# Performance work log

Hardware: AMD Instinct MI355X
Metric: run time of the kernel (lower is better)

The kernel has to match this reference:

```python
import jax, jax.numpy as jnp
import numpy as np

N_NODES = 100000
N_REL = 8
N_EDGES = 400000
D = 128
N_LAYERS = 3
NEG_SLOPE = 0.2


def setup_inputs() -> dict:
    key = jax.random.key(0)
    ks = jax.random.split(key, 8)
    scale = 0.05
    return {
        "h": jax.random.normal(ks[0], (N_NODES, D), dtype=jnp.float32),
        "edge_src": jax.random.randint(ks[1], (N_REL, N_EDGES), 0, N_NODES, dtype=jnp.int32),
        "edge_dst": jax.random.randint(ks[2], (N_REL, N_EDGES), 0, N_NODES, dtype=jnp.int32),
        "fc_src_w": jax.random.normal(ks[3], (N_LAYERS, N_REL, D, D), dtype=jnp.float32) * scale,
        "fc_dst_w": jax.random.normal(ks[4], (N_LAYERS, N_REL, D, D), dtype=jnp.float32) * scale,
        "attn_l": jax.random.normal(ks[5], (N_LAYERS, N_REL, D), dtype=jnp.float32) * scale,
        "attn_r": jax.random.normal(ks[6], (N_LAYERS, N_REL, D), dtype=jnp.float32) * scale,
        "h_bias": jax.random.normal(ks[7], (N_LAYERS, D), dtype=jnp.float32) * scale,
    }


def _rel_graph_layer(x, edge_src, edge_dst, Wsrc, Wdst, al, ar, bias, apply_relu):
    """One RelGraphConvLayer: per-relation GATConv (1 head) summed across relations."""
    n = x.shape[0]
    out = jnp.zeros((n, Wsrc.shape[-2]), dtype=x.dtype)
    for r in range(edge_src.shape[0]):
        src, dst = edge_src[r], edge_dst[r]
        zs = x @ Wsrc[r].T                      # [N, D] fc_src projection
        zd = x @ Wdst[r].T                      # [N, D] fc_dst projection
        el = zs @ al[r]                         # [N]
        er = zd @ ar[r]                         # [N]
        e = jax.nn.leaky_relu(el[src] + er[dst], NEG_SLOPE)  # [E]
        # edge softmax over incoming edges per dst node (stable)
        m = jax.ops.segment_max(e, dst, num_segments=n)
        w = jnp.exp(e - m[dst])
        denom = jax.ops.segment_sum(w, dst, num_segments=n)
        alpha = w / denom[dst]                  # [E]
        msg = zs[src] * alpha[:, None]          # [E, D]
        out = out + jax.ops.segment_sum(msg, dst, num_segments=n)
    out = out + bias
    if apply_relu:
        out = jax.nn.relu(out)
    return out  # mean over single head dim is a no-op


def reference(h, edge_src, edge_dst, fc_src_w, fc_dst_w, attn_l, attn_r, h_bias):
    x = h
    for l in range(N_LAYERS):
        x = _rel_graph_layer(
            x, edge_src, edge_dst,
            fc_src_w[l], fc_dst_w[l], attn_l[l], attn_r[l], h_bias[l],
            apply_relu=(l < N_LAYERS - 1),
        )
    return x
```

## Files before the change

kernel.cpp:

```cpp
#include <hip/hip_runtime.h>

#define NN 100000
#define NE 400000
#define NR 8
#define DD 128
#define NBK 391
#define BCAP 1536
#define P1B 32
#define NNP 100096

typedef unsigned short ushort_t;
using short8  = __attribute__((ext_vector_type(8))) short;
using f32x4   = __attribute__((ext_vector_type(4))) float;

__device__ __forceinline__ ushort_t f2bf(float f) {
  union { float f; unsigned u; } v; v.f = f;
  unsigned u = v.u;
  return (ushort_t)((u + 0x7FFFu + ((u >> 16) & 1u)) >> 16);
}
__device__ __forceinline__ float bf2f(unsigned hs) {
  union { unsigned u; float f; } v; v.u = hs << 16;
  return v.f;
}

__global__ __launch_bounds__(256) void f32_to_bf16_kernel(const float* __restrict__ in,
                                                          ushort_t* __restrict__ out, int n4) {
  int t = blockIdx.x * 256 + threadIdx.x;
  if (t < n4) {
    float4 f = ((const float4*)in)[t];
    uint2 p;
    p.x = (unsigned)f2bf(f.x) | ((unsigned)f2bf(f.y) << 16);
    p.y = (unsigned)f2bf(f.z) | ((unsigned)f2bf(f.w) << 16);
    ((uint2*)out)[t] = p;
  }
}

__global__ __launch_bounds__(256) void wfrag_kernel(const float* __restrict__ in, uint4* __restrict__ out) {
  int t = blockIdx.x * 256 + threadIdx.x;
  int lane = t & 63;
  int nt = (t >> 6) & 7;
  int s  = (t >> 9) & 3;
  int kc = (t >> 11) & 7;
  int l  = t >> 14;
  int m16 = lane & 15, kq = lane >> 4;
  int o = nt * 16 + m16;
  int chunk = s * 4 + kq;
  const float* p = in + ((((size_t)l * 8 + kc) * 128 + o) * 128 + chunk * 8);
  uint4 v;
  v.x = (unsigned)f2bf(p[0]) | ((unsigned)f2bf(p[1]) << 16);
  v.y = (unsigned)f2bf(p[2]) | ((unsigned)f2bf(p[3]) << 16);
  v.z = (unsigned)f2bf(p[4]) | ((unsigned)f2bf(p[5]) << 16);
  v.w = (unsigned)f2bf(p[6]) | ((unsigned)f2bf(p[7]) << 16);
  out[t] = v;
}

__global__ __launch_bounds__(256) void bucket_kernel(const int* __restrict__ edge_dst,
                                                     const int* __restrict__ edge_src,
                                                     int* __restrict__ gcur, unsigned* __restrict__ E1) {
  __shared__ unsigned stage[NBK][32];
  __shared__ int lcnt[NBK];
  int r   = blockIdx.x >> 5;
  int blk = blockIdx.x & 31;
  int t = threadIdx.x;
  for (int i = t; i < NBK; i += 256) lcnt[i] = 0;
  __syncthreads();
  const int per = NE / P1B;
  int e0 = blk * per, e1 = e0 + per;
  const int* ed = edge_dst + (size_t)r * NE;
  const int* es = edge_src + (size_t)r * NE;
  int* gc = gcur + r * NBK;
  unsigned* E1r = E1 + (size_t)r * NBK * BCAP;
  for (int base = e0; base < e1; base += 4096) {
    int lim = min(base + 4096, e1);
    for (int e = base + t; e < lim; e += 256) {
      int d = ed[e];
      unsigned val = ((unsigned)es[e] << 8) | (unsigned)(d & 255);
      int b = d >> 8;
      int slot = atomicAdd(&lcnt[b], 1);
      if (slot < 32) stage[b][slot] = val;
      else {
        int p = atomicAdd(&gc[b], 1);
        if (p < BCAP) E1r[(size_t)b * BCAP + p] = val;
      }
    }
    __syncthreads();
    for (int b = t; b < NBK; b += 256) {
      int c = lcnt[b]; if (c > 32) c = 32;
      int nf = c & ~15;
      if (nf) {
        int p = atomicAdd(&gc[b], nf);
        for (int k = 0; k < nf; k++)
          if (p + k < BCAP) E1r[(size_t)b * BCAP + p + k] = stage[b][k];
        for (int k = nf; k < c; k++) stage[b][k - nf] = stage[b][k];
      }
      lcnt[b] = c - nf;
    }
    __syncthreads();
  }
  for (int b = t; b < NBK; b += 256) {
    int c = lcnt[b]; if (c > 32) c = 32;
    if (c) {
      int p = atomicAdd(&gc[b], c);
      for (int k = 0; k < c; k++)
        if (p + k < BCAP) E1r[(size_t)b * BCAP + p + k] = stage[b][k];
    }
  }
}

__global__ __launch_bounds__(256) void bscan_kernel(const int* __restrict__ gcur, int* __restrict__ bbase) {
  __shared__ int ps[256];
  int t = threadIdx.x;
  int vals[13];
  int s = 0;
#pragma unroll
  for (int i = 0; i < 13; i++) {
    int idx = t * 13 + i;
    int c = (idx < NR * NBK) ? min(gcur[idx], BCAP) : 0;
    vals[i] = s; s += c;
  }
  ps[t] = s;
  __syncthreads();
  for (int off = 1; off < 256; off <<= 1) {
    int x = (t >= off) ? ps[t - off] : 0;
    __syncthreads();
    ps[t] += x;
    __syncthreads();
  }
  int excl = ps[t] - s;
#pragma unroll
  for (int i = 0; i < 13; i++) {
    int idx = t * 13 + i;
    if (idx < NR * NBK) bbase[idx] = excl + vals[i];
  }
}

__global__ __launch_bounds__(256) void csr_kernel(const unsigned* __restrict__ E1, const int* __restrict__ gcur,
                                                  const int* __restrict__ bbase,
                                                  int* __restrict__ offs, int* __restrict__ srcs) {
  __shared__ unsigned ent[BCAP];
  __shared__ int cnt[256], pref[256], excl_s[256];
  int rb = blockIdx.x;
  int b = rb % NBK, r = rb / NBK;
  int t = threadIdx.x;
  int n = min(gcur[rb], BCAP);
  const unsigned* src = E1 + (size_t)rb * BCAP;
  for (int i = t; i < n; i += 256) ent[i] = src[i];
  cnt[t] = 0;
  __syncthreads();
  for (int i = t; i < n; i += 256) atomicAdd(&cnt[ent[i] & 255], 1);
  __syncthreads();
  int v = cnt[t];
  pref[t] = v;
  __syncthreads();
  for (int off = 1; off < 256; off <<= 1) {
    int x = (t >= off) ? pref[t - off] : 0;
    __syncthreads();
    pref[t] += x;
    __syncthreads();
  }
  int excl = pref[t] - v;
  excl_s[t] = excl;
  int gb = bbase[rb];
  int d = b * 256 + t;
  if (d < NN) offs[(size_t)r * NN + d] = gb + excl;
  if (rb == NR * NBK - 1 && t == 0) offs[(size_t)NR * NN] = NR * NE;
  cnt[t] = 0;
  __syncthreads();
  for (int i = t; i < n; i += 256) {
    unsigned e = ent[i];
    int dl = e & 255;
    int p = atomicAdd(&cnt[dl], 1);
    srcs[gb + excl_s[dl] + p] = (int)(e >> 8);
  }
}

__global__ __launch_bounds__(128) void uv_all_kernel(const float* __restrict__ Wsrc, const float* __restrict__ Wdst,
                                                     const float* __restrict__ al, const float* __restrict__ ar,
                                                     ushort_t* __restrict__ uvb) {
  int rl = blockIdx.x, j = threadIdx.x;
  int l = rl >> 3, r = rl & 7;
  const float* Ws = Wsrc + (size_t)rl * DD * DD;
  const float* Wd = Wdst + (size_t)rl * DD * DD;
  float su = 0.f, sv = 0.f;
  for (int i = 0; i < DD; i++) {
    su += al[rl * DD + i] * Ws[i * DD + j];
    sv += ar[rl * DD + i] * Wd[i * DD + j];
  }
  uvb[((size_t)l * 16 + r) * DD + j]     = f2bf(su);
  uvb[((size_t)l * 16 + 8 + r) * DD + j] = f2bf(sv);
}

__global__ __launch_bounds__(256) void elr_kernel(const ushort_t* __restrict__ xb,
                                                  const ushort_t* __restrict__ uvb,
                                                  float* __restrict__ elr) {
  int t = threadIdx.x;
  int lane = t & 63, wave = t >> 6;
  int m16 = lane & 15, kq = lane >> 4;
  int n0 = blockIdx.x * 64 + wave * 16;
  const short8* Ag = (const short8*)xb;
  const short8* Bg = (const short8*)uvb;
  int bbase = m16 * 16 + kq;
  short8 b0 = Bg[bbase + 0];
  short8 b1 = Bg[bbase + 4];
  short8 b2 = Bg[bbase + 8];
  short8 b3 = Bg[bbase + 12];
  size_t abase = (size_t)(n0 + m16) * 16 + kq;
  short8 a0 = Ag[abase + 0];
  short8 a1 = Ag[abase + 4];
  short8 a2 = Ag[abase + 8];
  short8 a3 = Ag[abase + 12];
  f32x4 acc = (f32x4)(0.f);
  acc = __builtin_amdgcn_mfma_f32_16x16x32_bf16(a0, b0, acc, 0, 0, 0);
  acc = __builtin_amdgcn_mfma_f32_16x16x32_bf16(a1, b1, acc, 0, 0, 0);
  acc = __builtin_amdgcn_mfma_f32_16x16x32_bf16(a2, b2, acc, 0, 0, 0);
  acc = __builtin_amdgcn_mfma_f32_16x16x32_bf16(a3, b3, acc, 0, 0, 0);
#pragma unroll
  for (int i = 0; i < 4; i++) {
    int n = n0 + kq * 4 + i;
    if (n < NN) elr[(size_t)m16 * NN + n] = acc[i];
  }
}

#define GACC(J, P, W) { g##J[0] += (W) * bf2f((P).x & 0xffffu); g##J[1] += (W) * bf2f((P).x >> 16); \
                        g##J[2] += (W) * bf2f((P).y & 0xffffu); g##J[3] += (W) * bf2f((P).y >> 16); \
                        g##J[4] += (W) * bf2f((P).z & 0xffffu); g##J[5] += (W) * bf2f((P).z >> 16); \
                        g##J[6] += (W) * bf2f((P).w & 0xffffu); g##J[7] += (W) * bf2f((P).w >> 16); }

__global__ __launch_bounds__(256, 4) void agg_gemm_kernel(
    const int* __restrict__ srcs, const int* __restrict__ offs,
    const float* __restrict__ el, const float* __restrict__ er,
    const ushort_t* __restrict__ xin, const uint4* __restrict__ Wfrag,
    const float* __restrict__ bias, ushort_t* __restrict__ xout,
    float* __restrict__ dout, int relu, int last) {
  int t = threadIdx.x;
  int lane = t & 63, wave = t >> 6;
  int m16 = lane & 15, kq = lane >> 4;
  int row0 = blockIdx.x * 64;
  int n = row0 + wave * 16 + m16;
  const uint4* xk = (const uint4*)xin + kq;
  f32x4 acc[8];
#pragma unroll
  for (int nt = 0; nt < 8; nt++) acc[nt] = (f32x4)(0.f);

#pragma unroll 1
  for (int kc = 0; kc < NR; kc++) {
    float g0[8], g1[8], g2[8], g3[8];
#pragma unroll
    for (int c = 0; c < 8; c++) { g0[c] = 0.f; g1[c] = 0.f; g2[c] = 0.f; g3[c] = 0.f; }
    if (n < NN) {
      int k0 = offs[(size_t)kc * NN + n], k1 = offs[(size_t)kc * NN + n + 1];
      if (k1 > k0) {
        float erd = er[(size_t)kc * NN + n];
        const float* elv = el + (size_t)kc * NN;
        float denom = 0.f;
        for (int e = k0; e < k1; e += 2) {
          int s0 = srcs[e];
          int s1 = srcs[(e + 1 < k1) ? e + 1 : e];
          const uint4* q0 = xk + (size_t)s0 * 16;
          const uint4* q1 = xk + (size_t)s1 * 16;
          uint4 p00 = q0[0], p01 = q0[4], p02 = q0[8], p03 = q0[12];
          uint4 p10 = q1[0], p11 = q1[4], p12 = q1[8], p13 = q1[12];
          float x0 = elv[s0] + erd;
          float x1 = elv[s1] + erd;
          x0 = fmaxf(x0, 0.2f * x0);
          x1 = fmaxf(x1, 0.2f * x1);
          float w0 = __expf(x0);
          float w1 = (e + 1 < k1) ? __expf(x1) : 0.f;
          denom += w0 + w1;
          GACC(0, p00, w0) GACC(1, p01, w0) GACC(2, p02, w0) GACC(3, p03, w0)
          GACC(0, p10, w1) GACC(1, p11, w1) GACC(2, p12, w1) GACC(3, p13, w1)
        }
        float inv = 1.f / denom;
#pragma unroll
        for (int c = 0; c < 8; c++) { g0[c] *= inv; g1[c] *= inv; g2[c] *= inv; g3[c] *= inv; }
      }
    }
    short8 af[4];
#pragma unroll
    for (int c = 0; c < 8; c++) {
      af[0][c] = (short)f2bf(g0[c]);
      af[1][c] = (short)f2bf(g1[c]);
      af[2][c] = (short)f2bf(g2[c]);
      af[3][c] = (short)f2bf(g3[c]);
    }
    const uint4* wfp = Wfrag + (size_t)kc * 2048 + lane;
#pragma unroll
    for (int s = 0; s < 4; s++) {
#pragma unroll
      for (int nt = 0; nt < 8; nt++) {
        short8 bf = *reinterpret_cast<const short8*>(wfp + (s * 8 + nt) * 64);
        acc[nt] = __builtin_amdgcn_mfma_f32_16x16x32_bf16(af[s], bf, acc[nt], 0, 0, 0);
      }
    }
  }
#pragma unroll
  for (int i = 0; i < 4; i++) {
    int row = row0 + wave * 16 + kq * 4 + i;
    if (row < NN) {
#pragma unroll
      for (int nt = 0; nt < 8; nt++) {
        float vv = acc[nt][i] + bias[m16 + 16 * nt];
        if (relu) vv = fmaxf(vv, 0.f);
        if (last) dout[(size_t)row * DD + m16 + 16 * nt] = vv;
        else      xout[(size_t)row * DD + m16 + 16 * nt] = f2bf(vv);
      }
    }
  }
}

extern "C" void kernel_launch(void* const* d_in, const int* in_sizes, int n_in,
                              void* d_out, int out_size, void* d_ws, size_t ws_size,
                              hipStream_t stream) {
  const float* h        = (const float*)d_in[0];
  const int*   edge_src = (const int*)d_in[1];
  const int*   edge_dst = (const int*)d_in[2];
  const float* fc_src_w = (const float*)d_in[3];
  const float* fc_dst_w = (const float*)d_in[4];
  const float* attn_l   = (const float*)d_in[5];
  const float* attn_r   = (const float*)d_in[6];
  const float* h_bias   = (const float*)d_in[7];
  float* dout = (float*)d_out;
  (void)in_sizes; (void)n_in; (void)out_size; (void)ws_size;

  char* base = (char*)d_ws;
  size_t off = 0;
  auto alloc = [&](size_t bytes) -> void* {
    void* p = base + off;
    off += (bytes + 255) & ~(size_t)255;
    return p;
  };
  ushort_t* xb0   = (ushort_t*)alloc((size_t)NNP * DD * 2);
  ushort_t* xb1   = (ushort_t*)alloc((size_t)NNP * DD * 2);
  float*    ELR   = (float*)   alloc((size_t)16 * NN * 4);
  ushort_t* uvb   = (ushort_t*)alloc((size_t)3 * 16 * DD * 2);
  uint4*    Wfrag = (uint4*)   alloc((size_t)3 * NR * 4 * 8 * 64 * 16);
  int*      offs  = (int*)     alloc(((size_t)NR * NN + 1) * 4);
  unsigned* E1    = (unsigned*)alloc((size_t)NR * NBK * BCAP * 4);
  int*      gcur  = (int*)     alloc((size_t)NR * NBK * 4);
  int*      bbase = (int*)     alloc((size_t)NR * NBK * 4);
  int*      srcs  = (int*)     alloc((size_t)NR * NE * 4);

  (void)hipMemsetAsync(gcur, 0, (size_t)NR * NBK * 4, stream);
  (void)hipMemsetAsync(xb0 + (size_t)NN * DD, 0, (size_t)(NNP - NN) * DD * 2, stream);
  (void)hipMemsetAsync(xb1 + (size_t)NN * DD, 0, (size_t)(NNP - NN) * DD * 2, stream);
  bucket_kernel<<<NR * P1B, 256, 0, stream>>>(edge_dst, edge_src, gcur, E1);
  bscan_kernel<<<1, 256, 0, stream>>>(gcur, bbase);
  csr_kernel<<<NR * NBK, 256, 0, stream>>>(E1, gcur, bbase, offs, srcs);

  f32_to_bf16_kernel<<<(NN * DD / 4 + 255) / 256, 256, 0, stream>>>(h, xb0, NN * DD / 4);
  wfrag_kernel<<<3 * NR * 4 * 8 * 64 / 256, 256, 0, stream>>>(fc_src_w, Wfrag);
  uv_all_kernel<<<3 * NR, 128, 0, stream>>>(fc_src_w, fc_dst_w, attn_l, attn_r, uvb);

  const float* el = ELR;
  const float* er = ELR + (size_t)8 * NN;
  for (int l = 0; l < 3; l++) {
    ushort_t* xin  = (l & 1) ? xb1 : xb0;
    ushort_t* xout = (l & 1) ? xb0 : xb1;
    elr_kernel<<<(NN + 63) / 64, 256, 0, stream>>>(xin, uvb + (size_t)l * 16 * DD, ELR);
    agg_gemm_kernel<<<(NN + 63) / 64, 256, 0, stream>>>(
        srcs, offs, el, er, xin, Wfrag + (size_t)l * NR * 4 * 8 * 64,
        h_bias + (size_t)l * DD, xout, dout, (l < 2) ? 1 : 0, (l == 2) ? 1 : 0);
  }
}
```

Measured before the change: 1.111 ms.

## Split fused aggregate+GEMM into separate edge-gather and MFMA GEMM kernels

The fused aggregation/GEMM kernel is replaced by two kernels. An edge kernel gives each (node, relation) pair 16 lanes, which compute the softmax-weighted gather and write bf16 aggregates in MFMA fragment layout to a scratch buffer. A GEMM kernel then processes two 16-row tiles per wave, sharing each weight fragment load. This buys parallelism across relations and better gather coalescing at the cost of an extra round trip to global memory for the aggregates. The E1 and aggregate buffers now share scratch space, and a single x buffer is used in place.

```diff
diff --git a/kernel.cpp b/kernel.cpp
--- a/kernel.cpp
+++ b/kernel.cpp
@@ -8,6 +8,7 @@
 #define BCAP 1536
 #define P1B 32
 #define NNP 100096
+#define NTILE 6250
 
 typedef unsigned short ushort_t;
 using short8  = __attribute__((ext_vector_type(8))) short;
@@ -221,67 +222,74 @@
   }
 }
 
-#define GACC(J, P, W) { g##J[0] += (W) * bf2f((P).x & 0xffffu); g##J[1] += (W) * bf2f((P).x >> 16); \
-                        g##J[2] += (W) * bf2f((P).y & 0xffffu); g##J[3] += (W) * bf2f((P).y >> 16); \
-                        g##J[4] += (W) * bf2f((P).z & 0xffffu); g##J[5] += (W) * bf2f((P).z >> 16); \
-                        g##J[6] += (W) * bf2f((P).w & 0xffffu); g##J[7] += (W) * bf2f((P).w >> 16); }
-
-__global__ __launch_bounds__(256, 4) void agg_gemm_kernel(
-    const int* __restrict__ srcs, const int* __restrict__ offs,
-    const float* __restrict__ el, const float* __restrict__ er,
-    const ushort_t* __restrict__ xin, const uint4* __restrict__ Wfrag,
+__global__ __launch_bounds__(256) void edge_kernel(const int* __restrict__ srcs, const int* __restrict__ offs,
+                                                   const float* __restrict__ el, const float* __restrict__ er,
+                                                   const ushort_t* __restrict__ xb, uint4* __restrict__ agg) {
+  int t = threadIdx.x;
+  int lane16 = t & 15;
+  int id = blockIdx.x * 16 + (t >> 4);
+  int n = id % NN;
+  int rg = id / NN;
+  int k0 = offs[(size_t)rg * NN + n], k1 = offs[(size_t)rg * NN + n + 1];
+  float acc[8];
+#pragma unroll
+  for (int i = 0; i < 8; i++) acc[i] = 0.f;
+  if (k1 > k0) {
+    float erd = er[(size_t)rg * NN + n];
+    const float* elr = el + (size_t)rg * NN;
+    float denom = 0.f;
+    for (int e = k0; e < k1; e++) {
+      int s = srcs[e];
+      float x = elr[s] + erd;
+      x = x > 0.f ? x : 0.2f * x;
+      float w = __expf(x);
+      denom += w;
+      uint4 p = ((const uint4*)(xb + (size_t)s * DD))[lane16];
+      acc[0] += w * bf2f(p.x & 0xffffu);
+      acc[1] += w * bf2f(p.x >> 16);
+      acc[2] += w * bf2f(p.y & 0xffffu);
+      acc[3] += w * bf2f(p.y >> 16);
+      acc[4] += w * bf2f(p.z & 0xffffu);
+      acc[5] += w * bf2f(p.z >> 16);
+      acc[6] += w * bf2f(p.w & 0xffffu);
+      acc[7] += w * bf2f(p.w >> 16);
+    }
+    float inv = 1.f / denom;
+#pragma unroll
+    for (int i = 0; i < 8; i++) acc[i] *= inv;
+  }
+  uint4 o;
+  o.x = (unsigned)f2bf(acc[0]) | ((unsigned)f2bf(acc[1]) << 16);
+  o.y = (unsigned)f2bf(acc[2]) | ((unsigned)f2bf(acc[3]) << 16);
+  o.z = (unsigned)f2bf(acc[4]) | ((unsigned)f2bf(acc[5]) << 16);
+  o.w = (unsigned)f2bf(acc[6]) | ((unsigned)f2bf(acc[7]) << 16);
+  agg[((size_t)(n >> 4) * NR + rg) * 256 + (size_t)lane16 * 16 + (n & 15)] = o;
+}
+
+__global__ __launch_bounds__(256) void gemm2_kernel(
+    const uint4* __restrict__ AGG, const uint4* __restrict__ Wfrag,
     const float* __restrict__ bias, ushort_t* __restrict__ xout,
     float* __restrict__ dout, int relu, int last) {
   int t = threadIdx.x;
   int lane = t & 63, wave = t >> 6;
+  int gw = blockIdx.x * 4 + wave;
+  if (gw >= NTILE / 2) return;
   int m16 = lane & 15, kq = lane >> 4;
-  int row0 = blockIdx.x * 64;
-  int n = row0 + wave * 16 + m16;
-  const uint4* xk = (const uint4*)xin + kq;
-  f32x4 acc[8];
-#pragma unroll
-  for (int nt = 0; nt < 8; nt++) acc[nt] = (f32x4)(0.f);
-
+  float bv[8];
+#pragma unroll
+  for (int nt = 0; nt < 8; nt++) bv[nt] = bias[m16 + 16 * nt];
+  const uint4* ab0 = AGG + (size_t)(2 * gw) * (NR * 256);
+  const uint4* ab1 = ab0 + NR * 256;
+  f32x4 acc0[8], acc1[8];
+#pragma unroll
+  for (int nt = 0; nt < 8; nt++) { acc0[nt] = (f32x4)(0.f); acc1[nt] = (f32x4)(0.f); }
 #pragma unroll 1
   for (int kc = 0; kc < NR; kc++) {
-    float g0[8], g1[8], g2[8], g3[8];
-#pragma unroll
-    for (int c = 0; c < 8; c++) { g0[c] = 0.f; g1[c] = 0.f; g2[c] = 0.f; g3[c] = 0.f; }
-    if (n < NN) {
-      int k0 = offs[(size_t)kc * NN + n], k1 = offs[(size_t)kc * NN + n + 1];
-      if (k1 > k0) {
-        float erd = er[(size_t)kc * NN + n];
-        const float* elv = el + (size_t)kc * NN;
-        float denom = 0.f;
-        for (int e = k0; e < k1; e += 2) {
-          int s0 = srcs[e];
-          int s1 = srcs[(e + 1 < k1) ? e + 1 : e];
-          const uint4* q0 = xk + (size_t)s0 * 16;
-          const uint4* q1 = xk + (size_t)s1 * 16;
-          uint4 p00 = q0[0], p01 = q0[4], p02 = q0[8], p03 = q0[12];
-          uint4 p10 = q1[0], p11 = q1[4], p12 = q1[8], p13 = q1[12];
-          float x0 = elv[s0] + erd;
-          float x1 = elv[s1] + erd;
-          x0 = fmaxf(x0, 0.2f * x0);
-          x1 = fmaxf(x1, 0.2f * x1);
-          float w0 = __expf(x0);
-          float w1 = (e + 1 < k1) ? __expf(x1) : 0.f;
-          denom += w0 + w1;
-          GACC(0, p00, w0) GACC(1, p01, w0) GACC(2, p02, w0) GACC(3, p03, w0)
-          GACC(0, p10, w1) GACC(1, p11, w1) GACC(2, p12, w1) GACC(3, p13, w1)
-        }
-        float inv = 1.f / denom;
-#pragma unroll
-        for (int c = 0; c < 8; c++) { g0[c] *= inv; g1[c] *= inv; g2[c] *= inv; g3[c] *= inv; }
-      }
-    }
-    short8 af[4];
-#pragma unroll
-    for (int c = 0; c < 8; c++) {
-      af[0][c] = (short)f2bf(g0[c]);
-      af[1][c] = (short)f2bf(g1[c]);
-      af[2][c] = (short)f2bf(g2[c]);
-      af[3][c] = (short)f2bf(g3[c]);
+    short8 a0[4], a1[4];
+#pragma unroll
+    for (int s = 0; s < 4; s++) {
+      a0[s] = *reinterpret_cast<const short8*>(ab0 + kc * 256 + s * 64 + lane);
+      a1[s] = *reinterpret_cast<const short8*>(ab1 + kc * 256 + s * 64 + lane);
     }
     const uint4* wfp = Wfrag + (size_t)kc * 2048 + lane;
 #pragma unroll
@@ -289,20 +297,27 @@
 #pragma unroll
       for (int nt = 0; nt < 8; nt++) {
         short8 bf = *reinterpret_cast<const short8*>(wfp + (s * 8 + nt) * 64);
-        acc[nt] = __builtin_amdgcn_mfma_f32_16x16x32_bf16(af[s], bf, acc[nt], 0, 0, 0);
+        acc0[nt] = __builtin_amdgcn_mfma_f32_16x16x32_bf16(a0[s], bf, acc0[nt], 0, 0, 0);
+        acc1[nt] = __builtin_amdgcn_mfma_f32_16x16x32_bf16(a1[s], bf, acc1[nt], 0, 0, 0);
       }
     }
   }
+  int r0 = 2 * gw * 16 + kq * 4;
 #pragma unroll
   for (int i = 0; i < 4; i++) {
-    int row = row0 + wave * 16 + kq * 4 + i;
-    if (row < NN) {
-#pragma unroll
-      for (int nt = 0; nt < 8; nt++) {
-        float vv = acc[nt][i] + bias[m16 + 16 * nt];
-        if (relu) vv = fmaxf(vv, 0.f);
-        if (last) dout[(size_t)row * DD + m16 + 16 * nt] = vv;
-        else      xout[(size_t)row * DD + m16 + 16 * nt] = f2bf(vv);
+    int rowa = r0 + i, rowb = r0 + 16 + i;
+#pragma unroll
+    for (int nt = 0; nt < 8; nt++) {
+      float va = acc0[nt][i] + bv[nt];
+      float vb = acc1[nt][i] + bv[nt];
+      if (relu) { va = fmaxf(va, 0.f); vb = fmaxf(vb, 0.f); }
+      int col = m16 + 16 * nt;
+      if (last) {
+        dout[(size_t)rowa * DD + col] = va;
+        dout[(size_t)rowb * DD + col] = vb;
+      } else {
+        xout[(size_t)rowa * DD + col] = f2bf(va);
+        xout[(size_t)rowb * DD + col] = f2bf(vb);
       }
     }
   }
@@ -329,36 +344,37 @@
     off += (bytes + 255) & ~(size_t)255;
     return p;
   };
-  ushort_t* xb0   = (ushort_t*)alloc((size_t)NNP * DD * 2);
-  ushort_t* xb1   = (ushort_t*)alloc((size_t)NNP * DD * 2);
+  ushort_t* xb    = (ushort_t*)alloc((size_t)NNP * DD * 2);
   float*    ELR   = (float*)   alloc((size_t)16 * NN * 4);
   ushort_t* uvb   = (ushort_t*)alloc((size_t)3 * 16 * DD * 2);
   uint4*    Wfrag = (uint4*)   alloc((size_t)3 * NR * 4 * 8 * 64 * 16);
   int*      offs  = (int*)     alloc(((size_t)NR * NN + 1) * 4);
-  unsigned* E1    = (unsigned*)alloc((size_t)NR * NBK * BCAP * 4);
   int*      gcur  = (int*)     alloc((size_t)NR * NBK * 4);
   int*      bbase = (int*)     alloc((size_t)NR * NBK * 4);
   int*      srcs  = (int*)     alloc((size_t)NR * NE * 4);
+  size_t e1_bytes  = (size_t)NR * NBK * BCAP * 4;
+  size_t agg_bytes = (size_t)NTILE * NR * 256 * 16;
+  void* scratch = alloc(agg_bytes > e1_bytes ? agg_bytes : e1_bytes);
+  unsigned* E1  = (unsigned*)scratch;
+  uint4*    AGG = (uint4*)scratch;
 
   (void)hipMemsetAsync(gcur, 0, (size_t)NR * NBK * 4, stream);
-  (void)hipMemsetAsync(xb0 + (size_t)NN * DD, 0, (size_t)(NNP - NN) * DD * 2, stream);
-  (void)hipMemsetAsync(xb1 + (size_t)NN * DD, 0, (size_t)(NNP - NN) * DD * 2, stream);
+  (void)hipMemsetAsync(xb + (size_t)NN * DD, 0, (size_t)(NNP - NN) * DD * 2, stream);
   bucket_kernel<<<NR * P1B, 256, 0, stream>>>(edge_dst, edge_src, gcur, E1);
   bscan_kernel<<<1, 256, 0, stream>>>(gcur, bbase);
   csr_kernel<<<NR * NBK, 256, 0, stream>>>(E1, gcur, bbase, offs, srcs);
 
-  f32_to_bf16_kernel<<<(NN * DD / 4 + 255) / 256, 256, 0, stream>>>(h, xb0, NN * DD / 4);
+  f32_to_bf16_kernel<<<(NN * DD / 4 + 255) / 256, 256, 0, stream>>>(h, xb, NN * DD / 4);
   wfrag_kernel<<<3 * NR * 4 * 8 * 64 / 256, 256, 0, stream>>>(fc_src_w, Wfrag);
   uv_all_kernel<<<3 * NR, 128, 0, stream>>>(fc_src_w, fc_dst_w, attn_l, attn_r, uvb);
 
   const float* el = ELR;
   const float* er = ELR + (size_t)8 * NN;
   for (int l = 0; l < 3; l++) {
-    ushort_t* xin  = (l & 1) ? xb1 : xb0;
-    ushort_t* xout = (l & 1) ? xb0 : xb1;
-    elr_kernel<<<(NN + 63) / 64, 256, 0, stream>>>(xin, uvb + (size_t)l * 16 * DD, ELR);
-    agg_gemm_kernel<<<(NN + 63) / 64, 256, 0, stream>>>(
-        srcs, offs, el, er, xin, Wfrag + (size_t)l * NR * 4 * 8 * 64,
-        h_bias + (size_t)l * DD, xout, dout, (l < 2) ? 1 : 0, (l == 2) ? 1 : 0);
-  }
-}
+    elr_kernel<<<(NN + 63) / 64, 256, 0, stream>>>(xb, uvb + (size_t)l * 16 * DD, ELR);
+    edge_kernel<<<NN * NR / 16, 256, 0, stream>>>(srcs, offs, el, er, xb, AGG);
+    gemm2_kernel<<<(NTILE / 2 + 3) / 4, 256, 0, stream>>>(
+        AGG, Wfrag + (size_t)l * NR * 4 * 8 * 64, h_bias + (size_t)l * DD,
+        xb, dout, (l < 2) ? 1 : 0, (l == 2) ? 1 : 0);
+  }
+}
```

New measurement: 910.6 us. 1.22x faster.
